# Kernel optimization log

Measured on AMD Instinct MI355X. Metric: run time of the kernel, lower is better.

## Reference

```python
import jax, jax.numpy as jnp
import numpy as np

EPS = 1e-5
KS = 3  # deformable kernel size
K2 = KS * KS


def conv2d(x, w, stride=1, padding=1):
    return jax.lax.conv_general_dilated(
        x, w, window_strides=(stride, stride),
        padding=[(padding, padding), (padding, padding)],
        dimension_numbers=("NCHW", "OIHW", "NCHW"))


def batchnorm(x, gamma, beta):
    # training-mode BN: batch statistics over (N, H, W)
    mean = jnp.mean(x, axis=(0, 2, 3), keepdims=True)
    var = jnp.var(x, axis=(0, 2, 3), keepdims=True)
    xhat = (x - mean) * jax.lax.rsqrt(var + EPS)
    return xhat * gamma[None, :, None, None] + beta[None, :, None, None]


def deform_conv(x, offsets, w, pad=1):
    # x: (B,C,H,W); offsets: (B,2*K2,H,W) -> first K2 channels = row (y)
    # offsets, next K2 = col (x) offsets; w: (O,C,KS,KS)
    B, C, H, W = x.shape
    xp = jnp.pad(x, ((0, 0), (0, 0), (pad, pad), (pad, pad)))
    Hp, Wp = H + 2 * pad, W + 2 * pad
    # base grid (center of each output pixel in padded coords)
    p0_y = jnp.arange(H, dtype=x.dtype) + pad            # (H,)
    p0_x = jnp.arange(W, dtype=x.dtype) + pad            # (W,)
    # kernel tap offsets in [-1, 0, 1]^2, row-major
    pn = jnp.stack(jnp.meshgrid(jnp.arange(KS) - pad, jnp.arange(KS) - pad,
                                indexing="ij"), axis=-1).reshape(K2, 2).astype(x.dtype)
    off = offsets.reshape(B, 2, K2, H, W)
    off_y = jnp.transpose(off[:, 0], (0, 2, 3, 1))       # (B,H,W,K2)
    off_x = jnp.transpose(off[:, 1], (0, 2, 3, 1))
    py = p0_y[None, :, None, None] + pn[:, 0][None, None, None, :] + off_y
    px = p0_x[None, None, :, None] + pn[:, 1][None, None, None, :] + off_x
    py = jnp.clip(py, 0.0, Hp - 1.0)
    px = jnp.clip(px, 0.0, Wp - 1.0)
    y0 = jnp.floor(py).astype(jnp.int32)
    x0 = jnp.floor(px).astype(jnp.int32)
    y1 = jnp.minimum(y0 + 1, Hp - 1)
    x1 = jnp.minimum(x0 + 1, Wp - 1)
    wy = (py - y0.astype(x.dtype))[:, None]              # (B,1,H,W,K2)
    wx = (px - x0.astype(x.dtype))[:, None]

    def gather(xb, yi, xi):                              # xb (C,Hp,Wp)
        return xb[:, yi, xi]                             # (C,H,W,K2)
    g = jax.vmap(gather)
    v00 = g(xp, y0, x0)
    v01 = g(xp, y0, x1)
    v10 = g(xp, y1, x0)
    v11 = g(xp, y1, x1)
    sampled = (v00 * (1 - wy) * (1 - wx) + v01 * (1 - wy) * wx +
               v10 * wy * (1 - wx) + v11 * wy * wx)      # (B,C,H,W,K2)
    return jnp.einsum("bchwk,ock->bohw", sampled, w.reshape(w.shape[0], C, K2))


def setup_inputs() -> dict:
    key = jax.random.key(0)
    ks = jax.random.split(key, 16)
    B, Cin, P, H, W = 64, 64, 64, 64, 64
    s = lambda k, shp, fan: jax.random.normal(k, shp, jnp.float32) * (fan ** -0.5)
    return {
        "x": jax.random.normal(ks[0], (B, Cin, H, W), jnp.float32),
        "conv1_w": s(ks[1], (P, Cin, 3, 3), Cin * 9),
        "bn1_g": jnp.ones((P,), jnp.float32), "bn1_b": jnp.zeros((P,), jnp.float32),
        "conv2_w": s(ks[2], (16, P, 1, 1), P),
        "bn2_g": jnp.ones((16,), jnp.float32), "bn2_b": jnp.zeros((16,), jnp.float32),
        "off_w": s(ks[3], (18, 16, 3, 3), 16 * 9) * 0.1,
        "off_b": jnp.zeros((18,), jnp.float32),
        "conv3_w": s(ks[4], (16, 16, 3, 3), 16 * 9),
        "bn3_g": jnp.ones((16,), jnp.float32), "bn3_b": jnp.zeros((16,), jnp.float32),
        "conv4_w": s(ks[5], (P, 16, 3, 3), 16 * 9),
        "bn4_g": jnp.ones((P,), jnp.float32), "bn4_b": jnp.zeros((P,), jnp.float32),
    }


def reference(x, conv1_w, bn1_g, bn1_b, conv2_w, bn2_g, bn2_b, off_w, off_b,
              conv3_w, bn3_g, bn3_b, conv4_w, bn4_g, bn4_b):
    out = jax.nn.relu(batchnorm(conv2d(x, conv1_w, 1, 1), bn1_g, bn1_b))
    out = jax.nn.relu(batchnorm(conv2d(out, conv2_w, 1, 0), bn2_g, bn2_b))
    offsets = conv2d(out, off_w, 1, 1) + off_b[None, :, None, None]
    out = jax.nn.relu(batchnorm(deform_conv(out, offsets, conv3_w), bn3_g, bn3_b))
    out = batchnorm(conv2d(out, conv4_w, 1, 1), bn4_g, bn4_b)
    out = out + x  # identity shortcut (stride=1, in_planes==planes)
    return jax.nn.relu(out)
```

## Files before the change

### kernel.cpp

```cpp
#include <hip/hip_runtime.h>

#define BN_N 262144.0f

typedef unsigned short u16;
typedef __attribute__((ext_vector_type(8))) short short8;
typedef __attribute__((ext_vector_type(4))) float floatx4;

#define RP1 4224
#define IS1 278784
#define RP2 1584
#define IS2 104544
#define H2P_TOTAL 6690816

static __device__ __forceinline__ u16 f2bf(float f) {
  union { float f; unsigned u; } v; v.f = f;
  unsigned u = v.u;
  return (u16)((u + 0x7FFFu + ((u >> 16) & 1u)) >> 16);
}
static __device__ __forceinline__ float bf2f(u16 h) {
  union { unsigned u; float f; } v; v.u = ((unsigned)h) << 16;
  return v.f;
}
static __device__ __forceinline__ void cp16(const u16* g, u16* l) {
  __builtin_amdgcn_global_load_lds((const __attribute__((address_space(1))) unsigned int*)g,
                                   (__attribute__((address_space(3))) unsigned int*)l, 16, 0, 0);
}

__global__ __launch_bounds__(256) void prep_w_k(const float* __restrict__ w1,
                                                u16* __restrict__ Bsw) {
  int d = blockIdx.x * 256 + threadIdx.x;
  int kin = d & 7, n = (d >> 3) & 63, kgrp = (d >> 9) & 3, kc = d >> 11;
  int k = kc * 32 + kgrp * 8 + kin;
  int tap = k >> 6, c = k & 63;
  Bsw[d] = f2bf(w1[n * 576 + c * 9 + tap]);
}

__global__ __launch_bounds__(256) void prep_w4_k(const float* __restrict__ w4,
                                                 u16* __restrict__ Bsw4) {
  int d = blockIdx.x * 256 + threadIdx.x;
  if (d >= 10240) return;
  int kin = d & 7, n = (d >> 3) & 63, lk = (d >> 9) & 3, kk = d >> 11;
  int tap = kk * 2 + (lk >> 1);
  int c = ((lk & 1) << 3) + kin;
  float v = (tap < 9) ? w4[n * 144 + c * 9 + tap] : 0.f;
  Bsw4[d] = f2bf(v);
}

__global__ __launch_bounds__(256) void prep_w3_k(const float* __restrict__ w3,
                                                 u16* __restrict__ Bsw3) {
  int d = blockIdx.x * 256 + threadIdx.x;
  if (d >= 2560) return;
  int kin = d & 7, n = (d >> 3) & 15, lk = (d >> 7) & 3, kk = d >> 9;
  int k = kk * 32 + lk * 8 + kin;
  int tap = k >> 4, c = k & 15;
  float v = (tap < 9) ? w3[n * 144 + c * 9 + tap] : 0.f;
  Bsw3[d] = f2bf(v);
}

__global__ __launch_bounds__(256) void prep_wo_k(const float* __restrict__ ow,
                                                 u16* __restrict__ BswO) {
  int d = blockIdx.x * 256 + threadIdx.x;
  if (d >= 5120) return;
  int kin = d & 7, n = (d >> 3) & 31, lk = (d >> 8) & 3, kk = d >> 10;
  int tap = kk * 2 + (lk >> 1);
  int c = ((lk & 1) << 3) + kin;
  float v = (tap < 9 && n < 18) ? ow[n * 144 + c * 9 + tap] : 0.f;
  BswO[d] = f2bf(v);
}

__global__ __launch_bounds__(256) void prep_x_k(const float* __restrict__ x,
                                                u16* __restrict__ xp) {
  int yp = blockIdx.x;
  int b = blockIdx.y;
  int tid = threadIdx.x;
  u16* rowbase = xp + (size_t)(b * 66 + yp) * RP1;
  if (yp == 0 || yp == 65) {
    for (int i = tid; i < RP1 / 4; i += 256)
      ((ushort4*)rowbase)[i] = make_ushort4(0, 0, 0, 0);
    return;
  }
  int y = yp - 1;
  __shared__ __align__(16) u16 s[64][72];
  for (int i = tid; i < 4096; i += 256) {
    int c = i >> 6, xx = i & 63;
    s[xx][c] = f2bf(x[((b * 64 + c) << 12) + (y << 6) + xx]);
  }
  if (tid < 128) {
    int c = tid & 63;
    int pxp = (tid >> 6) ? 65 : 0;
    rowbase[pxp * 64 + c] = 0;
  }
  __syncthreads();
  for (int j = tid; j < 512; j += 256) {
    int xx = j >> 3, chunk = j & 7;
    int pxp = xx + 1;
    int ph = chunk ^ (pxp & 7);
    *(short8*)(rowbase + pxp * 64 + ph * 8) = *(const short8*)(&s[xx][chunk * 8]);
  }
}

__global__ __launch_bounds__(256, 4) void conv1_mfma(const u16* __restrict__ xp,
                                                     const u16* __restrict__ Bsw,
                                                     u16* __restrict__ h1,
                                                     float* __restrict__ sum1, float* __restrict__ sq1) {
  const int tid = threadIdx.x;
  const int w = tid >> 6, l = tid & 63;
  const int lm = l & 15, lk = l >> 4;
  const int b = blockIdx.x >> 4;
  const int y0 = (blockIdx.x & 15) << 2;
  const int y = y0 + w;
  const u16* base = xp + ((size_t)b * 66 + y) * RP1;

  floatx4 acc[4][4];
#pragma unroll
  for (int mt = 0; mt < 4; ++mt)
#pragma unroll
    for (int nb = 0; nb < 4; ++nb)
      acc[mt][nb] = (floatx4){0.f, 0.f, 0.f, 0.f};

#pragma unroll
  for (int kk = 0; kk < 18; ++kk) {
    const int tap = kk >> 1;
    const int dy = (tap < 3) ? 0 : ((tap < 6) ? 1 : 2);
    const int dx = tap - dy * 3;
    const int chunk = ((kk & 1) << 2) + lk;
    const u16* rp = base + dy * RP1;
    short8 aF[4], bF[4];
    const u16* bp_ = Bsw + ((((kk) * 4 + lk) * 64) + lm) * 8;
    bF[0] = *(const short8*)(bp_);
    bF[1] = *(const short8*)(bp_ + 128);
    bF[2] = *(const short8*)(bp_ + 256);
    bF[3] = *(const short8*)(bp_ + 384);
#pragma unroll
    for (int mt = 0; mt < 4; ++mt) {
      int pxp = mt * 16 + lm + dx;
      int ph = chunk ^ (pxp & 7);
      aF[mt] = *(const short8*)(rp + pxp * 64 + ph * 8);
    }
#pragma unroll
    for (int mt = 0; mt < 4; ++mt)
#pragma unroll
      for (int nb = 0; nb < 4; ++nb)
        acc[mt][nb] = __builtin_amdgcn_mfma_f32_16x16x32_bf16(aF[mt], bF[nb], acc[mt][nb], 0, 0, 0);
  }

#pragma unroll
  for (int mt = 0; mt < 4; ++mt)
#pragma unroll
    for (int nb = 0; nb < 4; ++nb) {
      u16* dst = h1 + ((size_t)(b * 64 + nb * 16 + lm) << 12) + (y << 6) + mt * 16 + (lk << 2);
      floatx4 v = acc[mt][nb];
      *(ushort4*)dst = make_ushort4(f2bf(v.x), f2bf(v.y), f2bf(v.z), f2bf(v.w));
    }

  __shared__ float LS[256], LQ[256];
  float s[4], s2[4];
#pragma unroll
  for (int nb = 0; nb < 4; ++nb) {
    s[nb] = 0.f; s2[nb] = 0.f;
#pragma unroll
    for (int mt = 0; mt < 4; ++mt) {
      floatx4 a = acc[mt][nb];
      s[nb] += a.x + a.y + a.z + a.w;
      s2[nb] += a.x * a.x + a.y * a.y + a.z * a.z + a.w * a.w;
    }
    s[nb] += __shfl_xor(s[nb], 16, 64);  s[nb] += __shfl_xor(s[nb], 32, 64);
    s2[nb] += __shfl_xor(s2[nb], 16, 64); s2[nb] += __shfl_xor(s2[nb], 32, 64);
  }
  if (lk == 0) {
#pragma unroll
    for (int nb = 0; nb < 4; ++nb) { LS[w * 64 + nb * 16 + lm] = s[nb]; LQ[w * 64 + nb * 16 + lm] = s2[nb]; }
  }
  __syncthreads();
  if (tid < 64) atomicAdd(&sum1[tid], LS[tid] + LS[64 + tid] + LS[128 + tid] + LS[192 + tid]);
  else if (tid < 128) { int o = tid - 64; atomicAdd(&sq1[o], LQ[o] + LQ[64 + o] + LQ[128 + o] + LQ[192 + o]); }
}

__global__ __launch_bounds__(256) void conv2_k(const u16* __restrict__ h1,
                                               const float* __restrict__ w2,
                                               const float* __restrict__ sum1, const float* __restrict__ sq1,
                                               const float* __restrict__ g1, const float* __restrict__ b1,
                                               float* __restrict__ out,
                                               float* __restrict__ sum2, float* __restrict__ sq2) {
  __shared__ float s_wt[64 * 16];
  __shared__ float s_scale[64], s_shift[64];
  __shared__ float ls[4][16], lsq[4][16];
  int tid = threadIdx.x;
  for (int i = tid; i < 1024; i += 256) {
    int o = i >> 6, c = i & 63;
    s_wt[c * 16 + o] = w2[i];
  }
  if (tid < 64) {
    float m = sum1[tid] / BN_N;
    float var = sq1[tid] / BN_N - m * m;
    float sc = g1[tid] * rsqrtf(var + 1e-5f);
    s_scale[tid] = sc;
    s_shift[tid] = b1[tid] - m * sc;
  }
  __syncthreads();
  int p = blockIdx.x * 256 + tid;
  int b = p >> 12, r = p & 4095;
  const u16* src = h1 + ((size_t)b << 18) + r;
  float acc[16];
#pragma unroll
  for (int o = 0; o < 16; ++o) acc[o] = 0.f;
  for (int c = 0; c < 64; ++c) {
    float v = bf2f(src[c << 12]);
    v = fmaxf(v * s_scale[c] + s_shift[c], 0.f);
    const float* wp = &s_wt[c * 16];
    float4 w0 = *(const float4*)wp;
    float4 w1 = *(const float4*)(wp + 4);
    float4 w2v = *(const float4*)(wp + 8);
    float4 w3v = *(const float4*)(wp + 12);
    acc[0] += w0.x * v;  acc[1] += w0.y * v;  acc[2] += w0.z * v;  acc[3] += w0.w * v;
    acc[4] += w1.x * v;  acc[5] += w1.y * v;  acc[6] += w1.z * v;  acc[7] += w1.w * v;
    acc[8] += w2v.x * v; acc[9] += w2v.y * v; acc[10] += w2v.z * v; acc[11] += w2v.w * v;
    acc[12] += w3v.x * v; acc[13] += w3v.y * v; acc[14] += w3v.z * v; acc[15] += w3v.w * v;
  }
  float* dst = out + (size_t)p * 16;
#pragma unroll
  for (int c4 = 0; c4 < 4; ++c4)
    *(float4*)(dst + c4 * 4) = make_float4(acc[c4*4], acc[c4*4+1], acc[c4*4+2], acc[c4*4+3]);
  int lane = tid & 63, wv = tid >> 6;
#pragma unroll
  for (int o = 0; o < 16; ++o) {
    float s = acc[o], s2 = acc[o] * acc[o];
#pragma unroll
    for (int off = 32; off > 0; off >>= 1) {
      s += __shfl_down(s, off, 64);
      s2 += __shfl_down(s2, off, 64);
    }
    if (lane == 0) { ls[wv][o] = s; lsq[wv][o] = s2; }
  }
  __syncthreads();
  if (tid < 16) atomicAdd(&sum2[tid], ls[0][tid] + ls[1][tid] + ls[2][tid] + ls[3][tid]);
  else if (tid < 32) {
    int o = tid - 16;
    atomicAdd(&sq2[o], lsq[0][o] + lsq[1][o] + lsq[2][o] + lsq[3][o]);
  }
}

__global__ __launch_bounds__(256) void bnrelu2_k(const float* __restrict__ ws2,
                                                 const float* __restrict__ sum2, const float* __restrict__ sq2,
                                                 const float* __restrict__ g2, const float* __restrict__ b2,
                                                 u16* __restrict__ h2p) {
  __shared__ float s_scale[16], s_shift[16];
  int tid = threadIdx.x;
  if (tid < 16) {
    float m = sum2[tid] / BN_N;
    float var = sq2[tid] / BN_N - m * m;
    float sc = g2[tid] * rsqrtf(var + 1e-5f);
    s_scale[tid] = sc;
    s_shift[tid] = b2[tid] - m * sc;
  }
  __syncthreads();
  int p = blockIdx.x * 256 + tid;
  int b = p >> 12, r = p & 4095;
  int y = r >> 6, xx = r & 63;
  const float* src = ws2 + (size_t)p * 16;
  u16* dst = h2p + (size_t)(b * 66 + y + 1) * RP2 + (xx + 1) * 24;
#pragma unroll
  for (int c4 = 0; c4 < 4; ++c4) {
    float4 v = *(const float4*)(src + c4 * 4);
    u16 o0 = f2bf(fmaxf(v.x * s_scale[c4*4]   + s_shift[c4*4],   0.f));
    u16 o1 = f2bf(fmaxf(v.y * s_scale[c4*4+1] + s_shift[c4*4+1], 0.f));
    u16 o2 = f2bf(fmaxf(v.z * s_scale[c4*4+2] + s_shift[c4*4+2], 0.f));
    u16 o3 = f2bf(fmaxf(v.w * s_scale[c4*4+3] + s_shift[c4*4+3], 0.f));
    *(ushort4*)(dst + c4 * 4) = make_ushort4(o0, o1, o2, o3);
  }
}

__global__ __launch_bounds__(256) void offconv_mfma(const u16* __restrict__ h2p,
                                                    const u16* __restrict__ BswO,
                                                    const float* __restrict__ ob,
                                                    float* __restrict__ offs) {
  __shared__ __align__(16) u16 lA[9728];
  __shared__ __align__(16) u16 lB[5120];
  const int tid = threadIdx.x;
  const int w = tid >> 6, l = tid & 63;
  const int lm = l & 15, lk = l >> 4;
  const int b = blockIdx.x >> 4;
  const int y0 = (blockIdx.x & 15) << 2;
  const int y = y0 + w;
  const u16* src = h2p + ((size_t)b * 66 + y0) * RP2;
  for (int seg = w; seg < 19; seg += 4) cp16(src + seg * 512 + l * 8, lA + seg * 512);
  for (int seg = w; seg < 10; seg += 4) cp16(BswO + seg * 512 + l * 8, lB + seg * 512);
  __syncthreads();

  floatx4 acc[4][2];
#pragma unroll
  for (int mt = 0; mt < 4; ++mt)
#pragma unroll
    for (int nb = 0; nb < 2; ++nb)
      acc[mt][nb] = (floatx4){0.f, 0.f, 0.f, 0.f};

#pragma unroll
  for (int kk = 0; kk < 5; ++kk) {
    int tap = kk * 2 + (lk >> 1);
    if (tap > 8) tap = 8;
    const int dy = tap / 3, dx = tap - dy * 3;
    const int c0 = (lk & 1) << 3;
    const int rowoff = (w + dy) * RP2;
    short8 aF[4], bF[2];
#pragma unroll
    for (int mt = 0; mt < 4; ++mt)
      aF[mt] = *(const short8*)(lA + rowoff + (mt * 16 + lm + dx) * 24 + c0);
    const u16* bp = lB + (((kk * 4 + lk) * 32) + lm) * 8;
    bF[0] = *(const short8*)(bp);
    bF[1] = *(const short8*)(bp + 128);
#pragma unroll
    for (int mt = 0; mt < 4; ++mt)
#pragma unroll
      for (int nb = 0; nb < 2; ++nb)
        acc[mt][nb] = __builtin_amdgcn_mfma_f32_16x16x32_bf16(aF[mt], bF[nb], acc[mt][nb], 0, 0, 0);
  }

#pragma unroll
  for (int mt = 0; mt < 4; ++mt)
#pragma unroll
    for (int nb = 0; nb < 2; ++nb) {
      int oc = nb * 16 + lm;
      if (oc < 18) {
        float bias = ob[oc];
        floatx4 v = acc[mt][nb];
        v.x += bias; v.y += bias; v.z += bias; v.w += bias;
        float* dst = offs + (size_t)b * 73728 + (oc << 12) + (y << 6) + mt * 16 + (lk << 2);
        *(floatx4*)dst = v;
      }
    }
}

__global__ __launch_bounds__(256) void deform_mfma(const u16* __restrict__ h2p,
                                                   const float* __restrict__ offs,
                                                   const u16* __restrict__ Bsw3,
                                                   float* __restrict__ out,
                                                   float* __restrict__ sum3, float* __restrict__ sq3) {
  const int tid = threadIdx.x;
  const int w = tid >> 6, l = tid & 63;
  const int lm = l & 15, lk = l >> 4;
  const int pbase = blockIdx.x * 256 + w * 64;
  const int b = pbase >> 12;
  const u16* img = h2p + (size_t)b * IS2;
  const float* offp = offs + (size_t)b * 73728;

  short8 bf[5];
#pragma unroll
  for (int kk = 0; kk < 5; ++kk)
    bf[kk] = *(const short8*)(Bsw3 + (((kk * 4 + lk) * 16) + lm) * 8);

  floatx4 acc[4];
#pragma unroll
  for (int mt = 0; mt < 4; ++mt) acc[mt] = (floatx4){0.f, 0.f, 0.f, 0.f};

#pragma unroll
  for (int mt = 0; mt < 4; ++mt) {
    const int p = pbase + mt * 16 + lm;
    const int r = p & 4095;
    const int y = r >> 6, x = r & 63;
#pragma unroll
    for (int kk = 0; kk < 5; ++kk) {
      const int k0 = kk * 32 + lk * 8;
      int tap = k0 >> 4;
      const int c0 = k0 & 15;
      if (tap > 8) tap = 8;
      const int dy = tap / 3, dx = tap - dy * 3;
      float offy = offp[(tap << 12) + r];
      float offx = offp[((tap + 9) << 12) + r];
      float py = (float)(y + dy) + offy;
      float px = (float)(x + dx) + offx;
      py = fminf(fmaxf(py, 0.f), 65.f);
      px = fminf(fmaxf(px, 0.f), 65.f);
      float y0f = floorf(py), x0f = floorf(px);
      int y0 = (int)y0f, x0 = (int)x0f;
      int y1 = min(y0 + 1, 65), x1 = min(x0 + 1, 65);
      float wy = py - y0f, wx = px - x0f;
      float w00 = (1.f - wy) * (1.f - wx), w01 = (1.f - wy) * wx;
      float w10 = wy * (1.f - wx),         w11 = wy * wx;
      short8 v00 = *(const short8*)(img + (y0 * 66 + x0) * 24 + c0);
      short8 v01 = *(const short8*)(img + (y0 * 66 + x1) * 24 + c0);
      short8 v10 = *(const short8*)(img + (y1 * 66 + x0) * 24 + c0);
      short8 v11 = *(const short8*)(img + (y1 * 66 + x1) * 24 + c0);
      short8 a;
#pragma unroll
      for (int j = 0; j < 8; ++j) {
        float s = bf2f((u16)v00[j]) * w00 + bf2f((u16)v01[j]) * w01
                + bf2f((u16)v10[j]) * w10 + bf2f((u16)v11[j]) * w11;
        a[j] = (short)f2bf(s);
      }
      acc[mt] = __builtin_amdgcn_mfma_f32_16x16x32_bf16(a, bf[kk], acc[mt], 0, 0, 0);
    }
  }

  float s = 0.f, s2 = 0.f;
#pragma unroll
  for (int mt = 0; mt < 4; ++mt) {
    floatx4 a = acc[mt];
    s += a.x + a.y + a.z + a.w;
    s2 += a.x * a.x + a.y * a.y + a.z * a.z + a.w * a.w;
#pragma unroll
    for (int reg = 0; reg < 4; ++reg) {
      int pp = pbase + mt * 16 + lk * 4 + reg;
      out[(size_t)pp * 16 + lm] = acc[mt][reg];
    }
  }
  __shared__ float ls[4][16], lsq[4][16];
  s += __shfl_xor(s, 16, 64);  s += __shfl_xor(s, 32, 64);
  s2 += __shfl_xor(s2, 16, 64); s2 += __shfl_xor(s2, 32, 64);
  if (lk == 0) { ls[w][lm] = s; lsq[w][lm] = s2; }
  __syncthreads();
  if (tid < 16) atomicAdd(&sum3[tid], ls[0][tid] + ls[1][tid] + ls[2][tid] + ls[3][tid]);
  else if (tid < 32) {
    int o = tid - 16;
    atomicAdd(&sq3[o], lsq[0][o] + lsq[1][o] + lsq[2][o] + lsq[3][o]);
  }
}

__global__ __launch_bounds__(256) void bnrelu3_k(const float* __restrict__ wsd,
                                                 const float* __restrict__ sum3, const float* __restrict__ sq3,
                                                 const float* __restrict__ g3, const float* __restrict__ b3,
                                                 u16* __restrict__ h3p) {
  __shared__ float s_scale[16], s_shift[16];
  int tid = threadIdx.x;
  if (tid < 16) {
    float m = sum3[tid] / BN_N;
    float var = sq3[tid] / BN_N - m * m;
    float sc = g3[tid] * rsqrtf(var + 1e-5f);
    s_scale[tid] = sc;
    s_shift[tid] = b3[tid] - m * sc;
  }
  __syncthreads();
  int p = blockIdx.x * 256 + tid;
  int b = p >> 12, r = p & 4095;
  int y = r >> 6, xx = r & 63;
  const float* src = wsd + (size_t)p * 16;
  u16* dst = h3p + (size_t)(b * 66 + y + 1) * RP2 + (xx + 1) * 24;
#pragma unroll
  for (int c4 = 0; c4 < 4; ++c4) {
    float4 v = *(const float4*)(src + c4 * 4);
    u16 o0 = f2bf(fmaxf(v.x * s_scale[c4*4]   + s_shift[c4*4],   0.f));
    u16 o1 = f2bf(fmaxf(v.y * s_scale[c4*4+1] + s_shift[c4*4+1], 0.f));
    u16 o2 = f2bf(fmaxf(v.z * s_scale[c4*4+2] + s_shift[c4*4+2], 0.f));
    u16 o3 = f2bf(fmaxf(v.w * s_scale[c4*4+3] + s_shift[c4*4+3], 0.f));
    *(ushort4*)(dst + c4 * 4) = make_ushort4(o0, o1, o2, o3);
  }
}

__global__ __launch_bounds__(256) void conv4_mfma(const u16* __restrict__ h3p,
                                                  const u16* __restrict__ Bsw4,
                                                  u16* __restrict__ h4,
                                                  float* __restrict__ sum4, float* __restrict__ sq4) {
  __shared__ __align__(16) u16 lA[9728];
  __shared__ __align__(16) u16 lB[10240];
  const int tid = threadIdx.x;
  const int w = tid >> 6, l = tid & 63;
  const int lm = l & 15, lk = l >> 4;
  const int b = blockIdx.x >> 4;
  const int y0 = (blockIdx.x & 15) << 2;
  const int y = y0 + w;
  const u16* src = h3p + ((size_t)b * 66 + y0) * RP2;
  for (int seg = w; seg < 19; seg += 4) cp16(src + seg * 512 + l * 8, lA + seg * 512);
  for (int seg = w; seg < 20; seg += 4) cp16(Bsw4 + seg * 512 + l * 8, lB + seg * 512);
  __syncthreads();

  floatx4 acc[4][4];
#pragma unroll
  for (int mt = 0; mt < 4; ++mt)
#pragma unroll
    for (int nb = 0; nb < 4; ++nb)
      acc[mt][nb] = (floatx4){0.f, 0.f, 0.f, 0.f};

#pragma unroll
  for (int kk = 0; kk < 5; ++kk) {
    int tap = kk * 2 + (lk >> 1);
    if (tap > 8) tap = 8;
    const int dy = tap / 3, dx = tap - dy * 3;
    const int c0 = (lk & 1) << 3;
    const int rowoff = (w + dy) * RP2;
    short8 aF[4], bF[4];
#pragma unroll
    for (int mt = 0; mt < 4; ++mt)
      aF[mt] = *(const short8*)(lA + rowoff + (mt * 16 + lm + dx) * 24 + c0);
    const u16* bp = lB + (((kk * 4 + lk) * 64) + lm) * 8;
    bF[0] = *(const short8*)(bp);
    bF[1] = *(const short8*)(bp + 128);
    bF[2] = *(const short8*)(bp + 256);
    bF[3] = *(const short8*)(bp + 384);
#pragma unroll
    for (int mt = 0; mt < 4; ++mt)
#pragma unroll
      for (int nb = 0; nb < 4; ++nb)
        acc[mt][nb] = __builtin_amdgcn_mfma_f32_16x16x32_bf16(aF[mt], bF[nb], acc[mt][nb], 0, 0, 0);
  }

#pragma unroll
  for (int mt = 0; mt < 4; ++mt)
#pragma unroll
    for (int nb = 0; nb < 4; ++nb) {
      u16* dst = h4 + ((size_t)(b * 64 + nb * 16 + lm) << 12) + (y << 6) + mt * 16 + (lk << 2);
      floatx4 v = acc[mt][nb];
      *(ushort4*)dst = make_ushort4(f2bf(v.x), f2bf(v.y), f2bf(v.z), f2bf(v.w));
    }

  __syncthreads();
  float* LS = (float*)lA;
  float* LQ = LS + 256;
  float s[4], s2[4];
#pragma unroll
  for (int nb = 0; nb < 4; ++nb) {
    s[nb] = 0.f; s2[nb] = 0.f;
#pragma unroll
    for (int mt = 0; mt < 4; ++mt) {
      floatx4 a = acc[mt][nb];
      s[nb] += a.x + a.y + a.z + a.w;
      s2[nb] += a.x * a.x + a.y * a.y + a.z * a.z + a.w * a.w;
    }
    s[nb] += __shfl_xor(s[nb], 16, 64);  s[nb] += __shfl_xor(s[nb], 32, 64);
    s2[nb] += __shfl_xor(s2[nb], 16, 64); s2[nb] += __shfl_xor(s2[nb], 32, 64);
  }
  if (lk == 0) {
#pragma unroll
    for (int nb = 0; nb < 4; ++nb) { LS[w * 64 + nb * 16 + lm] = s[nb]; LQ[w * 64 + nb * 16 + lm] = s2[nb]; }
  }
  __syncthreads();
  if (tid < 64) atomicAdd(&sum4[tid], LS[tid] + LS[64 + tid] + LS[128 + tid] + LS[192 + tid]);
  else if (tid < 128) { int o = tid - 64; atomicAdd(&sq4[o], LQ[o] + LQ[64 + o] + LQ[128 + o] + LQ[192 + o]); }
}

__global__ __launch_bounds__(256) void final_k(const u16* __restrict__ h4,
                                               float* __restrict__ out,
                                               const float* __restrict__ x,
                                               const float* __restrict__ sum4, const float* __restrict__ sq4,
                                               const float* __restrict__ g4, const float* __restrict__ b4) {
  __shared__ float s_scale[64], s_shift[64];
  int tid = threadIdx.x;
  if (tid < 64) {
    float m = sum4[tid] / BN_N;
    float var = sq4[tid] / BN_N - m * m;
    float sc = g4[tid] * rsqrtf(var + 1e-5f);
    s_scale[tid] = sc;
    s_shift[tid] = b4[tid] - m * sc;
  }
  __syncthreads();
  int i = (blockIdx.x * 256 + tid) * 4;
  int c = (i >> 12) & 63;
  ushort4 q = *(const ushort4*)(h4 + i);
  float4 xv = *(const float4*)(x + i);
  float sc = s_scale[c], sh = s_shift[c];
  float4 v;
  v.x = fmaxf(bf2f(q.x) * sc + sh + xv.x, 0.f);
  v.y = fmaxf(bf2f(q.y) * sc + sh + xv.y, 0.f);
  v.z = fmaxf(bf2f(q.z) * sc + sh + xv.z, 0.f);
  v.w = fmaxf(bf2f(q.w) * sc + sh + xv.w, 0.f);
  *(float4*)(out + i) = v;
}

extern "C" void kernel_launch(void* const* d_in, const int* in_sizes, int n_in,
                              void* d_out, int out_size, void* d_ws, size_t ws_size,
                              hipStream_t stream) {
  const float* x  = (const float*)d_in[0];
  const float* w1 = (const float*)d_in[1];
  const float* g1 = (const float*)d_in[2];
  const float* b1 = (const float*)d_in[3];
  const float* w2 = (const float*)d_in[4];
  const float* g2 = (const float*)d_in[5];
  const float* b2 = (const float*)d_in[6];
  const float* ow = (const float*)d_in[7];
  const float* ob = (const float*)d_in[8];
  const float* w3 = (const float*)d_in[9];
  const float* g3 = (const float*)d_in[10];
  const float* b3 = (const float*)d_in[11];
  const float* w4 = (const float*)d_in[12];
  const float* g4 = (const float*)d_in[13];
  const float* b4 = (const float*)d_in[14];
  float* out = (float*)d_out;
  float* ws = (float*)d_ws;

  float* offs = ws;
  float* wsd  = offs + 4718592;
  float* ws2  = wsd + 4194304;
  float* h2pf = ws2 + 4194304;
  float* stats = h2pf + 4460544;
  float* sum1 = stats, *sq1 = stats + 64;
  float* sum2 = stats + 128, *sq2 = stats + 144;
  float* sum3 = stats + 160, *sq3 = stats + 176;
  float* sum4 = stats + 192, *sq4 = stats + 256;
  u16* xp   = (u16*)ws;
  u16* Bsw  = (u16*)(stats + 320);
  u16* Bsw4 = Bsw + 36864;
  u16* Bsw3 = Bsw4 + 10240;
  u16* BswO = Bsw3 + 2560;
  u16* h2p  = (u16*)h2pf;
  u16* h4   = (u16*)offs;
  u16* h1   = (u16*)out;

  hipMemsetAsync(stats, 0, 320 * sizeof(float), stream);
  hipMemsetAsync(h2p, 0, (size_t)H2P_TOTAL * sizeof(u16), stream);

  prep_w_k<<<144, 256, 0, stream>>>(w1, Bsw);
  prep_w4_k<<<40, 256, 0, stream>>>(w4, Bsw4);
  prep_w3_k<<<10, 256, 0, stream>>>(w3, Bsw3);
  prep_wo_k<<<20, 256, 0, stream>>>(ow, BswO);
  prep_x_k<<<dim3(66, 64), 256, 0, stream>>>(x, xp);
  conv1_mfma<<<1024, 256, 0, stream>>>(xp, Bsw, h1, sum1, sq1);
  conv2_k<<<1024, 256, 0, stream>>>(h1, w2, sum1, sq1, g1, b1, ws2, sum2, sq2);
  bnrelu2_k<<<1024, 256, 0, stream>>>(ws2, sum2, sq2, g2, b2, h2p);
  offconv_mfma<<<1024, 256, 0, stream>>>(h2p, BswO, ob, offs);
  deform_mfma<<<1024, 256, 0, stream>>>(h2p, offs, Bsw3, wsd, sum3, sq3);
  bnrelu3_k<<<1024, 256, 0, stream>>>(wsd, sum3, sq3, g3, b3, h2p );
  conv4_mfma<<<1024, 256, 0, stream>>>(h2p, Bsw4, h4, sum4, sq4);
  final_k<<<16384, 256, 0, stream>>>(h4, out, x, sum4, sq4, g4, b4);
}
```

Baseline: 358.8 us.

## Stage conv1 weights and input rows in LDS with a double-buffered row ring

conv1 is restructured so that each block handles a quarter of an image (16 rows) instead of 4 rows. The full weight matrix and a 5-slot ring of padded input row pairs are loaded into LDS through global_load_lds, and the next rows are prefetched while the current 4 rows are computed. Before, every block read A and B fragments straight from global memory and refetched overlapping halo rows. The grid drops from 1024 blocks to 256 and each block now uses about 160KB of LDS, so only one block fits per CU. That reduces occupancy and parallelism in exchange for data reuse and overlap.

```diff
diff --git a/kernel.cpp b/kernel.cpp
--- a/kernel.cpp
+++ b/kernel.cpp
@@ -99,77 +99,118 @@
   }
 }
 
-__global__ __launch_bounds__(256, 4) void conv1_mfma(const u16* __restrict__ xp,
+__global__ __launch_bounds__(256, 1) void conv1_mfma(const u16* __restrict__ xp,
                                                      const u16* __restrict__ Bsw,
                                                      u16* __restrict__ h1,
                                                      float* __restrict__ sum1, float* __restrict__ sq1) {
+  __shared__ __align__(16) u16 ring[43520];
+  __shared__ __align__(16) u16 lB[36864];
+  __shared__ float LSQ[512];
   const int tid = threadIdx.x;
   const int w = tid >> 6, l = tid & 63;
   const int lm = l & 15, lk = l >> 4;
-  const int b = blockIdx.x >> 4;
-  const int y0 = (blockIdx.x & 15) << 2;
-  const int y = y0 + w;
-  const u16* base = xp + ((size_t)b * 66 + y) * RP1;
-
-  floatx4 acc[4][4];
-#pragma unroll
-  for (int mt = 0; mt < 4; ++mt)
+  const int b = blockIdx.x >> 2;
+  const int quarter = blockIdx.x & 3;
+  const int c0 = quarter * 8;
+  const u16* xb = xp + (size_t)b * 66 * RP1;
+
+  for (int i = w; i < 72; i += 4) cp16(Bsw + i * 512 + l * 8, lB + i * 512);
+#pragma unroll
+  for (int c = 0; c < 3; ++c) {
+    const u16* src = xb + (size_t)(2 * (c0 + c)) * RP1;
+    u16* dst = ring + ((c0 + c) % 5) * 8704;
+    for (int s = w; s < 17; s += 4) cp16(src + s * 512 + l * 8, dst + s * 512);
+  }
+  asm volatile("s_waitcnt vmcnt(0)" ::: "memory");
+  __builtin_amdgcn_s_barrier();
+  __builtin_amdgcn_sched_barrier(0);
+
+  float ssum[4] = {0.f, 0.f, 0.f, 0.f}, sqsm[4] = {0.f, 0.f, 0.f, 0.f};
+
+#pragma unroll 1
+  for (int j = 0; j < 4; ++j) {
+    const int y0 = quarter * 16 + j * 4;
+    if (j < 3) {
+#pragma unroll
+      for (int c = 0; c < 2; ++c) {
+        const int ch = c0 + 2 * j + 3 + c;
+        const u16* src = xb + (size_t)(2 * ch) * RP1;
+        u16* dst = ring + (ch % 5) * 8704;
+        for (int s = w; s < 17; s += 4) cp16(src + s * 512 + l * 8, dst + s * 512);
+      }
+      __builtin_amdgcn_sched_barrier(0);
+    }
+
+    floatx4 acc[4][4];
+#pragma unroll
+    for (int mt = 0; mt < 4; ++mt)
+#pragma unroll
+      for (int nb = 0; nb < 4; ++nb)
+        acc[mt][nb] = (floatx4){0.f, 0.f, 0.f, 0.f};
+
+#pragma unroll
+    for (int kk = 0; kk < 18; ++kk) {
+      const int tap = kk >> 1;
+      const int dy = (tap < 3) ? 0 : ((tap < 6) ? 1 : 2);
+      const int dx = tap - dy * 3;
+      const int chunk16 = ((kk & 1) << 2) + lk;
+      const int pr = y0 + w + dy;
+      const u16* abase = ring + ((pr >> 1) % 5) * 8704 + (pr & 1) * 4224;
+      short8 aF[4], bF[4];
+      const u16* bp = lB + (((kk * 4 + lk) * 64) + lm) * 8;
+      bF[0] = *(const short8*)(bp);
+      bF[1] = *(const short8*)(bp + 128);
+      bF[2] = *(const short8*)(bp + 256);
+      bF[3] = *(const short8*)(bp + 384);
+#pragma unroll
+      for (int mt = 0; mt < 4; ++mt) {
+        int pxp = mt * 16 + lm + dx;
+        int ph = chunk16 ^ (pxp & 7);
+        aF[mt] = *(const short8*)(abase + pxp * 64 + ph * 8);
+      }
+#pragma unroll
+      for (int mt = 0; mt < 4; ++mt)
+#pragma unroll
+        for (int nb = 0; nb < 4; ++nb)
+          acc[mt][nb] = __builtin_amdgcn_mfma_f32_16x16x32_bf16(aF[mt], bF[nb], acc[mt][nb], 0, 0, 0);
+    }
+
+    const int y = y0 + w;
+#pragma unroll
+    for (int mt = 0; mt < 4; ++mt)
+#pragma unroll
+      for (int nb = 0; nb < 4; ++nb) {
+        u16* dst = h1 + ((size_t)(b * 64 + nb * 16 + lm) << 12) + (y << 6) + mt * 16 + (lk << 2);
+        floatx4 v = acc[mt][nb];
+        *(ushort4*)dst = make_ushort4(f2bf(v.x), f2bf(v.y), f2bf(v.z), f2bf(v.w));
+      }
+
 #pragma unroll
     for (int nb = 0; nb < 4; ++nb)
-      acc[mt][nb] = (floatx4){0.f, 0.f, 0.f, 0.f};
-
-#pragma unroll
-  for (int kk = 0; kk < 18; ++kk) {
-    const int tap = kk >> 1;
-    const int dy = (tap < 3) ? 0 : ((tap < 6) ? 1 : 2);
-    const int dx = tap - dy * 3;
-    const int chunk = ((kk & 1) << 2) + lk;
-    const u16* rp = base + dy * RP1;
-    short8 aF[4], bF[4];
-    const u16* bp_ = Bsw + ((((kk) * 4 + lk) * 64) + lm) * 8;
-    bF[0] = *(const short8*)(bp_);
-    bF[1] = *(const short8*)(bp_ + 128);
-    bF[2] = *(const short8*)(bp_ + 256);
-    bF[3] = *(const short8*)(bp_ + 384);
-#pragma unroll
-    for (int mt = 0; mt < 4; ++mt) {
-      int pxp = mt * 16 + lm + dx;
-      int ph = chunk ^ (pxp & 7);
-      aF[mt] = *(const short8*)(rp + pxp * 64 + ph * 8);
-    }
-#pragma unroll
-    for (int mt = 0; mt < 4; ++mt)
-#pragma unroll
-      for (int nb = 0; nb < 4; ++nb)
-        acc[mt][nb] = __builtin_amdgcn_mfma_f32_16x16x32_bf16(aF[mt], bF[nb], acc[mt][nb], 0, 0, 0);
-  }
-
-#pragma unroll
-  for (int mt = 0; mt < 4; ++mt)
-#pragma unroll
-    for (int nb = 0; nb < 4; ++nb) {
-      u16* dst = h1 + ((size_t)(b * 64 + nb * 16 + lm) << 12) + (y << 6) + mt * 16 + (lk << 2);
-      floatx4 v = acc[mt][nb];
-      *(ushort4*)dst = make_ushort4(f2bf(v.x), f2bf(v.y), f2bf(v.z), f2bf(v.w));
-    }
-
-  __shared__ float LS[256], LQ[256];
-  float s[4], s2[4];
+#pragma unroll
+      for (int mt = 0; mt < 4; ++mt) {
+        floatx4 a = acc[mt][nb];
+        ssum[nb] += a.x + a.y + a.z + a.w;
+        sqsm[nb] += a.x * a.x + a.y * a.y + a.z * a.z + a.w * a.w;
+      }
+
+    if (j < 3) {
+      asm volatile("s_waitcnt vmcnt(16)" ::: "memory");
+      __builtin_amdgcn_s_barrier();
+      __builtin_amdgcn_sched_barrier(0);
+    }
+  }
+
+  float* LS = LSQ;
+  float* LQ = LSQ + 256;
 #pragma unroll
   for (int nb = 0; nb < 4; ++nb) {
-    s[nb] = 0.f; s2[nb] = 0.f;
-#pragma unroll
-    for (int mt = 0; mt < 4; ++mt) {
-      floatx4 a = acc[mt][nb];
-      s[nb] += a.x + a.y + a.z + a.w;
-      s2[nb] += a.x * a.x + a.y * a.y + a.z * a.z + a.w * a.w;
-    }
-    s[nb] += __shfl_xor(s[nb], 16, 64);  s[nb] += __shfl_xor(s[nb], 32, 64);
-    s2[nb] += __shfl_xor(s2[nb], 16, 64); s2[nb] += __shfl_xor(s2[nb], 32, 64);
+    ssum[nb] += __shfl_xor(ssum[nb], 16, 64);  ssum[nb] += __shfl_xor(ssum[nb], 32, 64);
+    sqsm[nb] += __shfl_xor(sqsm[nb], 16, 64);  sqsm[nb] += __shfl_xor(sqsm[nb], 32, 64);
   }
   if (lk == 0) {
 #pragma unroll
-    for (int nb = 0; nb < 4; ++nb) { LS[w * 64 + nb * 16 + lm] = s[nb]; LQ[w * 64 + nb * 16 + lm] = s2[nb]; }
+    for (int nb = 0; nb < 4; ++nb) { LS[w * 64 + nb * 16 + lm] = ssum[nb]; LQ[w * 64 + nb * 16 + lm] = sqsm[nb]; }
   }
   __syncthreads();
   if (tid < 64) atomicAdd(&sum1[tid], LS[tid] + LS[64 + tid] + LS[128 + tid] + LS[192 + tid]);
@@ -601,7 +642,7 @@
   prep_w3_k<<<10, 256, 0, stream>>>(w3, Bsw3);
   prep_wo_k<<<20, 256, 0, stream>>>(ow, BswO);
   prep_x_k<<<dim3(66, 64), 256, 0, stream>>>(x, xp);
-  conv1_mfma<<<1024, 256, 0, stream>>>(xp, Bsw, h1, sum1, sq1);
+  conv1_mfma<<<256, 256, 0, stream>>>(xp, Bsw, h1, sum1, sq1);
   conv2_k<<<1024, 256, 0, stream>>>(h1, w2, sum1, sq1, g1, b1, ws2, sum2, sq2);
   bnrelu2_k<<<1024, 256, 0, stream>>>(ws2, sum2, sq2, g2, b2, h2p);
   offconv_mfma<<<1024, 256, 0, stream>>>(h2p, BswO, ob, offs);
```

Measured after the change: 323.8 us. 9.8% less time.
